# Performance work log

Hardware: AMD Instinct MI355X
Metric: run time of the kernel (lower is better)

## Reference

```python
import jax, jax.numpy as jnp
import numpy as np


def setup_inputs() -> dict:
    key = jax.random.key(0)
    k1, k2 = jax.random.split(key)
    x = jax.random.normal(k1, (64, 32, 32, 128), dtype=jnp.float32)
    embeddings = jax.random.normal(k2, (128, 1024), dtype=jnp.float32)  # (embedding_dim, num_embeddings)
    return {"x": x, "embeddings": embeddings}


def reference(x, embeddings):
    d = embeddings.shape[0]
    flat = x.reshape(-1, d)  # [N, d]
    # squared L2 distances: ||f||^2 + ||e||^2 - 2 f.e
    similarity = flat @ embeddings  # [N, K]
    distances = (jnp.sum(flat * flat, axis=1, keepdims=True)
                 + jnp.sum(embeddings * embeddings, axis=0)
                 - 2.0 * similarity)
    idx = jnp.argmin(distances, axis=1)  # [N]
    # gather codes (equivalent to one_hot @ embeddings^T)
    quantized = embeddings.T[idx].reshape(x.shape)
    # straight-through estimator
    quantized = x + jax.lax.stop_gradient(quantized - x)
    return quantized
```

## Files before the change

### kernel.cpp

```cpp
#include <hip/hip_runtime.h>


#define NROWS 65536
#define DDIM 128
#define KCODES 1024
#define MARGIN1 0.004f

typedef __attribute__((ext_vector_type(8))) short short8;
typedef __attribute__((ext_vector_type(16))) float f32x16;

__device__ inline ushort f2bf(float f) {
    union { float f; unsigned u; } v; v.f = f;
    unsigned r = v.u + 0x7fffu + ((v.u >> 16) & 1u);
    return (ushort)(r >> 16);
}
__device__ inline float bf2f(ushort b) {
    union { unsigned u; float f; } v; v.u = ((unsigned)b) << 16;
    return v.f;
}

__global__ void k_transpose(const float* __restrict__ e, float* __restrict__ et) {
    int gid = blockIdx.x * blockDim.x + threadIdx.x;
    int d = gid >> 10, k = gid & 1023;
    et[k * DDIM + d] = e[gid];
}

__global__ void k_norms(const float* __restrict__ e, float* __restrict__ nrm,
                        double* __restrict__ nrm64) {
    int k = blockIdx.x * blockDim.x + threadIdx.x;
    double s = 0.0;
    for (int d = 0; d < DDIM; ++d) {
        double v = (double)e[d * KCODES + k];
        s = fma(v, v, s);
    }
    nrm64[k] = s; nrm[k] = (float)s;
}

__global__ void k_pack_e(const float* __restrict__ e, uint4* __restrict__ epq) {
    int t = blockIdx.x * blockDim.x + threadIdx.x;
    int lane = t & 63, c = (t >> 6) & 7, h = (t >> 9) & 1, nt = t >> 10;
    int col = nt * 32 + (lane & 31);
    int kbase = c * 16 + ((lane >> 5) << 3);
    union { ushort u[8]; uint4 q; } pk;
    #pragma unroll
    for (int j = 0; j < 8; ++j) {
        float v = e[(kbase + j) * KCODES + col];
        ushort hb = f2bf(v);
        pk.u[j] = (h == 0) ? hb : f2bf(v - bf2f(hb));
    }
    epq[(size_t)nt * 1024 + h * 512 + c * 64 + lane] = pk.q;
}

__global__ __launch_bounds__(256, 2) void k_argmin32(const float* __restrict__ x,
                                                     const uint4* __restrict__ epq,
                                                     const float* __restrict__ nrm,
                                                     int* __restrict__ idx,
                                                     int* __restrict__ wlc,
                                                     int* __restrict__ wl) {
    __shared__ uint4 sbuf[2][1024];

    const int tid = threadIdx.x;
    const int lane = tid & 63;
    const int w = tid >> 6;
    const int rt = blockIdx.x * 4 + w;
    const int lrow = lane & 31;
    const int lgrp = lane >> 5;

    const float* xr = x + (size_t)(rt * 32 + lrow) * DDIM + (lgrp << 3);
    short8 ah[8], al[8];
    #pragma unroll
    for (int c = 0; c < 8; ++c) {
        float4 u = *reinterpret_cast<const float4*>(xr + c * 16);
        float4 v = *reinterpret_cast<const float4*>(xr + c * 16 + 4);
        float fv[8] = {u.x, u.y, u.z, u.w, v.x, v.y, v.z, v.w};
        short8 hi, lo;
        #pragma unroll
        for (int j = 0; j < 8; ++j) {
            ushort hb = f2bf(fv[j]);
            hi[j] = (short)hb;
            lo[j] = (short)f2bf(fv[j] - bf2f(hb));
        }
        ah[c] = hi; al[c] = lo;
    }

    float b1[16], b2[16]; int bi[16];
    #pragma unroll
    for (int r = 0; r < 16; ++r) { b1[r] = 3.4e38f; b2[r] = 3.4e38f; bi[r] = 0; }

    uint4 st[4];
    #pragma unroll
    for (int i = 0; i < 4; ++i) st[i] = epq[i * 256 + tid];
    #pragma unroll
    for (int i = 0; i < 4; ++i) sbuf[0][i * 256 + tid] = st[i];

    int cur = 0;
    for (int t = 0; t < 32; ++t) {
        __syncthreads();
        if (t + 1 < 32) {
            #pragma unroll
            for (int i = 0; i < 4; ++i)
                st[i] = epq[(size_t)(t + 1) * 1024 + i * 256 + tid];
        }
        const float nv = nrm[t * 32 + lrow];
        const int code = t * 32 + lrow;

        f32x16 acc;
        #pragma unroll
        for (int r = 0; r < 16; ++r) acc[r] = 0.f;

        #pragma unroll
        for (int c = 0; c < 8; ++c) {
            union { uint4 q; short8 s; } bh, bl;
            bh.q = sbuf[cur][c * 64 + lane];
            bl.q = sbuf[cur][512 + c * 64 + lane];
            acc = __builtin_amdgcn_mfma_f32_32x32x16_bf16(ah[c], bh.s, acc, 0, 0, 0);
            acc = __builtin_amdgcn_mfma_f32_32x32x16_bf16(ah[c], bl.s, acc, 0, 0, 0);
            acc = __builtin_amdgcn_mfma_f32_32x32x16_bf16(al[c], bh.s, acc, 0, 0, 0);
        }
        if (t + 1 < 32) {
            #pragma unroll
            for (int i = 0; i < 4; ++i) sbuf[cur ^ 1][i * 256 + tid] = st[i];
        }

        #pragma unroll
        for (int r = 0; r < 16; ++r) {
            float s = fmaf(-2.f, acc[r], nv);
            bool lt = s < b1[r];
            b2[r] = lt ? b1[r] : fminf(b2[r], s);
            b1[r] = lt ? s : b1[r];
            bi[r] = lt ? code : bi[r];
        }
        cur ^= 1;
    }

    #pragma unroll
    for (int r = 0; r < 16; ++r) {
        #pragma unroll
        for (int m = 1; m < 32; m <<= 1) {
            float o1 = __shfl_xor(b1[r], m);
            float o2 = __shfl_xor(b2[r], m);
            int   oi = __shfl_xor(bi[r], m);
            bool take = (o1 < b1[r]) || (o1 == b1[r] && oi < bi[r]);
            float loser = take ? b1[r] : o1;
            b1[r] = take ? o1 : b1[r];
            bi[r] = take ? oi : bi[r];
            b2[r] = fminf(fminf(b2[r], o2), loser);
        }
    }

    if (lrow == 0) {
        #pragma unroll
        for (int r = 0; r < 16; ++r) {
            int rl = (r & 3) + 8 * (r >> 2) + 4 * lgrp;
            int row = rt * 32 + rl;
            idx[row] = bi[r];
            if (b2[r] - b1[r] < MARGIN1) {
                int slot = atomicAdd(wlc, 1);
                wl[slot] = row;
            }
        }
    }
}

__global__ __launch_bounds__(256) void k_fix(const float* __restrict__ x,
                                             const float* __restrict__ e,
                                             const double* __restrict__ nrm64,
                                             const int* __restrict__ wlc,
                                             const int* __restrict__ wl,
                                             int* __restrict__ idx) {
    __shared__ float  xs[DDIM];
    __shared__ double w1[4]; __shared__ double w2_[4]; __shared__ int wi[4];
    const int tid = threadIdx.x;
    const int lane = tid & 63;
    const int wv = tid >> 6;
    const int n = *wlc;

    for (int i = blockIdx.x; i < n; i += gridDim.x) {
        const int row = wl[i];
        if (tid < DDIM) xs[tid] = x[(size_t)row * DDIM + tid];
        __syncthreads();

        double dot[4] = {0.0, 0.0, 0.0, 0.0};
        for (int d0 = 0; d0 < DDIM; d0 += 8) {
            float ef[8][4];
            #pragma unroll
            for (int dd = 0; dd < 8; ++dd)
                #pragma unroll
                for (int kk = 0; kk < 4; ++kk)
                    ef[dd][kk] = e[(d0 + dd) * KCODES + tid + kk * 256];
            #pragma unroll
            for (int dd = 0; dd < 8; ++dd) {
                double xv = (double)xs[d0 + dd];
                #pragma unroll
                for (int kk = 0; kk < 4; ++kk)
                    dot[kk] = fma(xv, (double)ef[dd][kk], dot[kk]);
            }
        }

        double bb1 = 1e300, bb2 = 1e300; int bbi = 0;
        #pragma unroll
        for (int kk = 0; kk < 4; ++kk) {
            int k = tid + kk * 256;
            double sc = nrm64[k] - 2.0 * dot[kk];
            if (sc < bb1) { bb2 = bb1; bb1 = sc; bbi = k; }
            else if (sc < bb2) bb2 = sc;
        }
        #pragma unroll
        for (int m = 1; m < 64; m <<= 1) {
            double o1 = __shfl_xor(bb1, m);
            int    oi = __shfl_xor(bbi, m);
            bool take = (o1 < bb1) || (o1 == bb1 && oi < bbi);
            bb1 = take ? o1 : bb1;
            bbi = take ? oi : bbi;
        }
        if (lane == 0) { w1[wv] = bb1; wi[wv] = bbi; }
        __syncthreads();
        if (tid == 0) {
            double f1 = w1[0]; int fi = wi[0];
            #pragma unroll
            for (int j = 1; j < 4; ++j) {
                bool take = (w1[j] < f1) || (w1[j] == f1 && wi[j] < fi);
                f1 = take ? w1[j] : f1;
                fi = take ? wi[j] : fi;
            }
            idx[row] = fi;
        }
        __syncthreads();
    }
}

__global__ void k_gather(const float* __restrict__ x, const float* __restrict__ et,
                         const int* __restrict__ idxp, float* __restrict__ out) {
    int gid = blockIdx.x * blockDim.x + threadIdx.x;
    int row = gid >> 5, d4 = gid & 31;
    float4 q = reinterpret_cast<const float4*>(et)[(size_t)idxp[row] * 32 + d4];
    float4 xv = reinterpret_cast<const float4*>(x)[gid];
    float4 o;
    o.x = xv.x + (q.x - xv.x);
    o.y = xv.y + (q.y - xv.y);
    o.z = xv.z + (q.z - xv.z);
    o.w = xv.w + (q.w - xv.w);
    reinterpret_cast<float4*>(out)[gid] = o;
}

extern "C" void kernel_launch(void* const* d_in, const int* in_sizes, int n_in,
                              void* d_out, int out_size, void* d_ws, size_t ws_size,
                              hipStream_t stream) {
    const float* x = (const float*)d_in[0];
    const float* e = (const float*)d_in[1];
    float* out = (float*)d_out;

    double* nrm64 = (double*)d_ws;
    float*  et    = (float*)d_ws + 2048;
    float*  nrm   = et + 131072;
    int*    idx   = (int*)(nrm + 1024);
    int*    wlc   = idx + NROWS;
    int*    wl    = wlc + 4;
    uint4*  epq   = (uint4*)(wl + NROWS);

    hipMemsetAsync(wlc, 0, sizeof(int), stream);

    k_transpose<<<(KCODES * DDIM) / 256, 256, 0, stream>>>(e, et);
    k_norms<<<KCODES / 256, 256, 0, stream>>>(e, nrm, nrm64);
    k_pack_e<<<32768 / 256, 256, 0, stream>>>(e, epq);
    k_argmin32<<<NROWS / 128, 256, 0, stream>>>(x, epq, nrm, idx, wlc, wl);
    k_fix<<<64, 256, 0, stream>>>(x, e, nrm64, wlc, wl, idx);
    k_gather<<<(NROWS * 32) / 256, 256, 0, stream>>>(x, et, idx, out);
}
```

Measured before the change: 101.1 us.

## Split codebook across blocks, add merge kernel, fuse prep kernels, use direct LDS loads

Merges the transpose, norm and pack kernels into one prep launch, with the norm computation parallelised eight ways and reduced by shuffles. The argmin kernel now splits the 1024 codes into two halves handled by separate blocks, doubling the grid to 1024 blocks and raising the occupancy hint. Each block writes partial best/second-best results that a new merge kernel combines before building the fix worklist. Codebook tiles are staged through global_load_lds instead of register round-trips. The cost is that x is loaded and split into bf16 twice, plus extra partial-result traffic and one more launch.

```diff
diff --git a/kernel.cpp b/kernel.cpp
--- a/kernel.cpp
+++ b/kernel.cpp
@@ -19,52 +19,68 @@
     return v.f;
 }
 
-__global__ void k_transpose(const float* __restrict__ e, float* __restrict__ et) {
-    int gid = blockIdx.x * blockDim.x + threadIdx.x;
-    int d = gid >> 10, k = gid & 1023;
-    et[k * DDIM + d] = e[gid];
-}
-
-__global__ void k_norms(const float* __restrict__ e, float* __restrict__ nrm,
-                        double* __restrict__ nrm64) {
-    int k = blockIdx.x * blockDim.x + threadIdx.x;
-    double s = 0.0;
-    for (int d = 0; d < DDIM; ++d) {
-        double v = (double)e[d * KCODES + k];
-        s = fma(v, v, s);
-    }
-    nrm64[k] = s; nrm[k] = (float)s;
-}
-
-__global__ void k_pack_e(const float* __restrict__ e, uint4* __restrict__ epq) {
-    int t = blockIdx.x * blockDim.x + threadIdx.x;
-    int lane = t & 63, c = (t >> 6) & 7, h = (t >> 9) & 1, nt = t >> 10;
-    int col = nt * 32 + (lane & 31);
-    int kbase = c * 16 + ((lane >> 5) << 3);
-    union { ushort u[8]; uint4 q; } pk;
-    #pragma unroll
-    for (int j = 0; j < 8; ++j) {
-        float v = e[(kbase + j) * KCODES + col];
-        ushort hb = f2bf(v);
-        pk.u[j] = (h == 0) ? hb : f2bf(v - bf2f(hb));
-    }
-    epq[(size_t)nt * 1024 + h * 512 + c * 64 + lane] = pk.q;
-}
-
-__global__ __launch_bounds__(256, 2) void k_argmin32(const float* __restrict__ x,
+__device__ inline void gload_lds16(const uint4* g, uint4* lds) {
+    __builtin_amdgcn_global_load_lds((const __attribute__((address_space(1))) void*)g,
+                                     (__attribute__((address_space(3))) void*)lds,
+                                     16, 0, 0);
+}
+
+__global__ void k_prep(const float* __restrict__ e, float* __restrict__ et,
+                       float* __restrict__ nrm, double* __restrict__ nrm64,
+                       uint4* __restrict__ epq) {
+    const int gid = blockIdx.x * blockDim.x + threadIdx.x;
+
+    {
+        int d = gid >> 10, k = gid & 1023;
+        et[k * DDIM + d] = e[gid];
+    }
+
+    if (gid < 32768) {
+        int lane = gid & 63, c = (gid >> 6) & 7, h = (gid >> 9) & 1, nt = gid >> 10;
+        int col = nt * 32 + (lane & 31);
+        int kbase = c * 16 + ((lane >> 5) << 3);
+        union { ushort u[8]; uint4 q; } pk;
+        #pragma unroll
+        for (int j = 0; j < 8; ++j) {
+            float v = e[(kbase + j) * KCODES + col];
+            ushort hb = f2bf(v);
+            pk.u[j] = (h == 0) ? hb : f2bf(v - bf2f(hb));
+        }
+        epq[(size_t)nt * 1024 + h * 512 + c * 64 + lane] = pk.q;
+    }
+
+    if (gid >= 32768 && gid < 32768 + 8192) {
+        int t2 = gid - 32768;
+        int k = t2 >> 3, part = t2 & 7;
+        double s = 0.0;
+        #pragma unroll
+        for (int j = 0; j < 16; ++j) {
+            double v = (double)e[(part * 16 + j) * KCODES + k];
+            s = fma(v, v, s);
+        }
+        #pragma unroll
+        for (int m = 1; m < 8; m <<= 1) s += __shfl_xor(s, m);
+        if (part == 0) { nrm64[k] = s; nrm[k] = (float)s; }
+    }
+}
+
+__global__ __launch_bounds__(256, 4) void k_argmin32(const float* __restrict__ x,
                                                      const uint4* __restrict__ epq,
                                                      const float* __restrict__ nrm,
-                                                     int* __restrict__ idx,
-                                                     int* __restrict__ wlc,
-                                                     int* __restrict__ wl) {
+                                                     float* __restrict__ pb1,
+                                                     float* __restrict__ pb2,
+                                                     int* __restrict__ pbi) {
     __shared__ uint4 sbuf[2][1024];
 
     const int tid = threadIdx.x;
     const int lane = tid & 63;
     const int w = tid >> 6;
-    const int rt = blockIdx.x * 4 + w;
+    const int kh = blockIdx.x & 1;
+    const int rg = blockIdx.x >> 1;
+    const int rt = rg * 4 + w;
     const int lrow = lane & 31;
     const int lgrp = lane >> 5;
+    const int tbase = kh * 16;
 
     const float* xr = x + (size_t)(rt * 32 + lrow) * DDIM + (lgrp << 3);
     short8 ah[8], al[8];
@@ -87,22 +103,22 @@
     #pragma unroll
     for (int r = 0; r < 16; ++r) { b1[r] = 3.4e38f; b2[r] = 3.4e38f; bi[r] = 0; }
 
-    uint4 st[4];
-    #pragma unroll
-    for (int i = 0; i < 4; ++i) st[i] = epq[i * 256 + tid];
-    #pragma unroll
-    for (int i = 0; i < 4; ++i) sbuf[0][i * 256 + tid] = st[i];
+    #pragma unroll
+    for (int i = 0; i < 4; ++i)
+        gload_lds16(epq + (size_t)tbase * 1024 + i * 256 + tid,
+                    &sbuf[0][i * 256 + (w << 6)]);
+    __syncthreads();
 
     int cur = 0;
-    for (int t = 0; t < 32; ++t) {
-        __syncthreads();
-        if (t + 1 < 32) {
+    for (int t = 0; t < 16; ++t) {
+        if (t + 1 < 16) {
             #pragma unroll
             for (int i = 0; i < 4; ++i)
-                st[i] = epq[(size_t)(t + 1) * 1024 + i * 256 + tid];
-        }
-        const float nv = nrm[t * 32 + lrow];
-        const int code = t * 32 + lrow;
+                gload_lds16(epq + (size_t)(tbase + t + 1) * 1024 + i * 256 + tid,
+                            &sbuf[cur ^ 1][i * 256 + (w << 6)]);
+        }
+        const int code = (tbase + t) * 32 + lrow;
+        const float nv = nrm[code];
 
         f32x16 acc;
         #pragma unroll
@@ -117,10 +133,6 @@
             acc = __builtin_amdgcn_mfma_f32_32x32x16_bf16(ah[c], bl.s, acc, 0, 0, 0);
             acc = __builtin_amdgcn_mfma_f32_32x32x16_bf16(al[c], bh.s, acc, 0, 0, 0);
         }
-        if (t + 1 < 32) {
-            #pragma unroll
-            for (int i = 0; i < 4; ++i) sbuf[cur ^ 1][i * 256 + tid] = st[i];
-        }
 
         #pragma unroll
         for (int r = 0; r < 16; ++r) {
@@ -130,6 +142,7 @@
             b1[r] = lt ? s : b1[r];
             bi[r] = lt ? code : bi[r];
         }
+        __syncthreads();
         cur ^= 1;
     }
 
@@ -152,13 +165,29 @@
         #pragma unroll
         for (int r = 0; r < 16; ++r) {
             int rl = (r & 3) + 8 * (r >> 2) + 4 * lgrp;
-            int row = rt * 32 + rl;
-            idx[row] = bi[r];
-            if (b2[r] - b1[r] < MARGIN1) {
-                int slot = atomicAdd(wlc, 1);
-                wl[slot] = row;
-            }
-        }
+            size_t o = (size_t)kh * NROWS + rt * 32 + rl;
+            pb1[o] = b1[r]; pb2[o] = b2[r]; pbi[o] = bi[r];
+        }
+    }
+}
+
+__global__ void k_merge(const float* __restrict__ pb1, const float* __restrict__ pb2,
+                        const int* __restrict__ pbi, int* __restrict__ idx,
+                        int* __restrict__ wlc, int* __restrict__ wl) {
+    int r = blockIdx.x * blockDim.x + threadIdx.x;
+    float a1 = pb1[r], a2 = pb2[r];
+    int   ai = pbi[r];
+    float c1 = pb1[NROWS + r], c2 = pb2[NROWS + r];
+    int   ci = pbi[NROWS + r];
+    bool take = c1 < a1;
+    float f1 = take ? c1 : a1;
+    int   fi = take ? ci : ai;
+    float loser = take ? a1 : c1;
+    float f2 = fminf(fminf(a2, c2), loser);
+    idx[r] = fi;
+    if (f2 - f1 < MARGIN1) {
+        int slot = atomicAdd(wlc, 1);
+        wl[slot] = r;
     }
 }
 
@@ -169,7 +198,7 @@
                                              const int* __restrict__ wl,
                                              int* __restrict__ idx) {
     __shared__ float  xs[DDIM];
-    __shared__ double w1[4]; __shared__ double w2_[4]; __shared__ int wi[4];
+    __shared__ double w1[4]; __shared__ int wi[4];
     const int tid = threadIdx.x;
     const int lane = tid & 63;
     const int wv = tid >> 6;
@@ -197,13 +226,12 @@
             }
         }
 
-        double bb1 = 1e300, bb2 = 1e300; int bbi = 0;
+        double bb1 = 1e300; int bbi = 0;
         #pragma unroll
         for (int kk = 0; kk < 4; ++kk) {
             int k = tid + kk * 256;
             double sc = nrm64[k] - 2.0 * dot[kk];
-            if (sc < bb1) { bb2 = bb1; bb1 = sc; bbi = k; }
-            else if (sc < bb2) bb2 = sc;
+            if (sc < bb1) { bb1 = sc; bbi = k; }
         }
         #pragma unroll
         for (int m = 1; m < 64; m <<= 1) {
@@ -257,13 +285,15 @@
     int*    wlc   = idx + NROWS;
     int*    wl    = wlc + 4;
     uint4*  epq   = (uint4*)(wl + NROWS);
+    float*  pb1   = (float*)(epq + 32768);
+    float*  pb2   = pb1 + 2 * NROWS;
+    int*    pbi   = (int*)(pb2 + 2 * NROWS);
 
     hipMemsetAsync(wlc, 0, sizeof(int), stream);
 
-    k_transpose<<<(KCODES * DDIM) / 256, 256, 0, stream>>>(e, et);
-    k_norms<<<KCODES / 256, 256, 0, stream>>>(e, nrm, nrm64);
-    k_pack_e<<<32768 / 256, 256, 0, stream>>>(e, epq);
-    k_argmin32<<<NROWS / 128, 256, 0, stream>>>(x, epq, nrm, idx, wlc, wl);
+    k_prep<<<512, 256, 0, stream>>>(e, et, nrm, nrm64, epq);
+    k_argmin32<<<1024, 256, 0, stream>>>(x, epq, nrm, pb1, pb2, pbi);
+    k_merge<<<NROWS / 256, 256, 0, stream>>>(pb1, pb2, pbi, idx, wlc, wl);
     k_fix<<<64, 256, 0, stream>>>(x, e, nrm64, wlc, wl, idx);
     k_gather<<<(NROWS * 32) / 256, 256, 0, stream>>>(x, et, idx, out);
 }
```

After: 123.4 us. 22.1% more time.
